# Kernel tuning notes

Measured on AMD Instinct MI355X. Metric: run time of the kernel, lower is better.

Reference implementation:

```python
import jax, jax.numpy as jnp
import numpy as np

B, C, H, W = 32, 512, 32, 32
R = C // 2  # reduced channels for key/prod projections


def setup_inputs() -> dict:
    key = jax.random.key(0)
    ks = jax.random.split(key, 8)
    s_in = 1.0 / np.sqrt(C)
    return {
        "x": jax.random.normal(ks[0], (B, C, H, W), jnp.float32),
        "Wk": jax.random.normal(ks[1], (R, C), jnp.float32) * s_in,
        "bk": jax.random.normal(ks[2], (R,), jnp.float32) * s_in,
        "Wp": jax.random.normal(ks[3], (R, C), jnp.float32) * s_in,
        "bp": jax.random.normal(ks[4], (R,), jnp.float32) * s_in,
        "Wv": jax.random.normal(ks[5], (C, C), jnp.float32) * s_in,
        "bv": jax.random.normal(ks[6], (C,), jnp.float32) * s_in,
        "param": jax.random.normal(ks[7], (1,), jnp.float32),
    }


def _conv1x1(x, Wmat, b):
    # 1x1 conv on NCHW == per-pixel channel matmul
    return jnp.einsum('bchw,oc->bohw', x, Wmat) + b[None, :, None, None]


def reference(x, Wk, bk, Wp, bp, Wv, bv, param):
    b, c, h, w = x.shape
    hw = h * w
    f_key = _conv1x1(x, Wk, bk).reshape(b, -1, hw).transpose(0, 2, 1)  # [B,HW,R]
    f_prod = _conv1x1(x, Wp, bp).reshape(b, -1, hw)                    # [B,R,HW]
    f_value = _conv1x1(x, Wv, bv).reshape(b, -1, hw)                   # [B,C,HW]
    energy = jnp.einsum('bnr,brm->bnm', f_key, f_prod)                 # [B,HW,HW]
    similarity = jax.nn.softmax(energy, axis=-1)
    # bmm(f_value, similarity^T): out[b,c,n] = sum_m f_value[b,c,m] * sim[b,n,m]
    attended = jnp.einsum('bcm,bnm->bcn', f_value, similarity).reshape(b, c, h, w)
    return x + attended * param
```

## Files before the change

kernel.cpp:

```cpp
#include <hip/hip_runtime.h>
#include <hip/hip_bf16.h>

#define BATCH 32
#define CCH   512
#define HWSZ  1024
#define RCH   256

typedef __attribute__((ext_vector_type(8))) _Float16 f16x8;
typedef __attribute__((ext_vector_type(4))) float f32x4;

__device__ __forceinline__ ushort f2h(float f) {
    _Float16 h = (_Float16)f;
    ushort u; __builtin_memcpy(&u, &h, 2);
    return u;
}
__device__ __forceinline__ float h2f(ushort u) {
    _Float16 h; __builtin_memcpy(&h, &u, 2);
    return (float)h;
}

__device__ __forceinline__ void load_lds16(const void* g, void* l) {
    __builtin_amdgcn_global_load_lds((const __attribute__((address_space(1))) void*)g,
                                     (__attribute__((address_space(3))) void*)l,
                                     16, 0, 0);
}

__device__ __forceinline__ void xcd_swizzle(int& bx, int& by, int& bz) {
    int gx = gridDim.x, gy = gridDim.y;
    int n   = gx * gy * gridDim.z;
    int lin = bx + gx * (by + gy * bz);
    int cpx = n >> 3;
    int s = (lin & 7) * cpx + (lin >> 3);
    bx = s % gx; s /= gx;
    by = s % gy;
    bz = s / gy;
}

__global__ __launch_bounds__(256) void k_prep_w(
    const float* __restrict__ Wk, const float* __restrict__ bk,
    const float* __restrict__ Wp, const float* __restrict__ bp,
    const float* __restrict__ Wv,
    ushort* __restrict__ Wkp_h, ushort* __restrict__ Wv_h, float* __restrict__ bias_kp)
{
    int idx = blockIdx.x * 256 + threadIdx.x;
    if (idx < 512 * 512) {
        int o = idx >> 9, c = idx & 511;
        float w = (o < 256) ? Wk[o * 512 + c] : Wp[(o - 256) * 512 + c];
        Wkp_h[idx] = f2h(w);
        Wv_h[idx]  = f2h(Wv[idx]);
        if (c == 0) bias_kp[o] = (o < 256) ? bk[o] : bp[o - 256];
    }
}

__global__ __launch_bounds__(256) void k_transpose(
    const float* __restrict__ x, ushort* __restrict__ xt)
{
    __shared__ float tile[64][65];
    int b  = blockIdx.z;
    int c0 = blockIdx.y * 64;
    int n0 = blockIdx.x * 64;
    const float* xb = x + (size_t)b * CCH * HWSZ;
    int t  = threadIdx.x;
    int tq = t >> 6;
    int tl = t & 63;
    #pragma unroll
    for (int i = 0; i < 16; ++i) {
        int c = i * 4 + tq;
        tile[c][tl] = xb[(size_t)(c0 + c) * HWSZ + n0 + tl];
    }
    __syncthreads();
    ushort* oh = xt + (size_t)b * HWSZ * CCH;
    #pragma unroll
    for (int i = 0; i < 16; ++i) {
        int n = i * 4 + tq;
        oh[(size_t)(n0 + n) * CCH + c0 + tl] = f2h(tile[tl][n]);
    }
}

template<int MODE>
__global__ __launch_bounds__(512, 2) void k_gemm8(
    const ushort* __restrict__ A, const ushort* __restrict__ B,
    int lda, int ldb, long aBatch, long bBatch,
    float* __restrict__ outF, ushort* __restrict__ out16,
    long oBatch, int ldo,
    const float* __restrict__ bias,
    const float* __restrict__ xres, const float* __restrict__ param,
    int NT)
{
    __shared__ ushort lds[2][2][2][8192];
    int bx = blockIdx.x, by = blockIdx.y, bz = blockIdx.z;
    xcd_swizzle(bx, by, bz);
    const int z  = bz;
    const int m0 = bx * 256;
    const int n0 = by * 256;
    const int t    = threadIdx.x;
    const int lane = t & 63;
    const int w    = t >> 6;
    const int wm = w >> 2, wn = w & 3;
    const int l15 = lane & 15;
    const int G   = (lane >> 4) ^ ((lane >> 1) & 3);

    const ushort* Ab = A + (size_t)z * aBatch;
    const ushort* Bb = B + (size_t)z * bBatch;

    const int sr = t >> 2;
    const int sg = (t & 3) ^ ((t >> 3) & 3);

    f32x4 acc[8][4] = {};
    f16x8 a[8], b[2];

#define STAGE(par, op, ks, kt) do {                                          \
        const ushort* gb_ = (op) ? Bb : Ab;                                  \
        int ld_ = (op) ? ldb : lda;                                          \
        int r0_ = (op) ? n0 : m0;                                            \
        size_t src_ = (size_t)(r0_ + sr) * ld_ + (kt) * 64 + (ks) * 32 + sg * 8; \
        load_lds16(gb_ + src_, &lds[par][op][ks][t * 8]);                    \
        load_lds16(gb_ + src_ + (size_t)128 * ld_, &lds[par][op][ks][t * 8 + 4096]); \
    } while (0)

#define LDA_(cur, ks) do {                                                   \
        _Pragma("unroll")                                                    \
        for (int mi = 0; mi < 8; ++mi)                                       \
            a[mi] = *(const f16x8*)&lds[cur][0][ks][(wm * 128 + mi * 16 + l15) * 32 + G * 8]; \
    } while (0)

#define LDB_(cur, ks, nh) do {                                               \
        _Pragma("unroll")                                                    \
        for (int ni = 0; ni < 2; ++ni)                                       \
            b[ni] = *(const f16x8*)&lds[cur][1][ks][(wn * 64 + (nh) * 32 + ni * 16 + l15) * 32 + G * 8]; \
    } while (0)

#define BAR() __builtin_amdgcn_s_barrier()

#define MFMA_BLK(nh) do {                                                    \
        asm volatile("s_waitcnt lgkmcnt(0)" ::: "memory");                   \
        __builtin_amdgcn_sched_barrier(0);                                   \
        __builtin_amdgcn_s_setprio(1);                                       \
        _Pragma("unroll")                                                    \
        for (int mi = 0; mi < 8; ++mi) {                                     \
            acc[mi][(nh)*2+0] = __builtin_amdgcn_mfma_f32_16x16x32_f16(a[mi], b[0], acc[mi][(nh)*2+0], 0, 0, 0); \
            acc[mi][(nh)*2+1] = __builtin_amdgcn_mfma_f32_16x16x32_f16(a[mi], b[1], acc[mi][(nh)*2+1], 0, 0, 0); \
        }                                                                    \
        __builtin_amdgcn_s_setprio(0);                                       \
    } while (0)

    STAGE(0, 0, 0, 0); STAGE(0, 1, 0, 0); STAGE(0, 0, 1, 0); STAGE(0, 1, 1, 0);
    asm volatile("s_waitcnt vmcnt(4)" ::: "memory");
    BAR();

    for (int j = 0; j < NT - 1; ++j) {
        int cur = j & 1, nxt = cur ^ 1;
        STAGE(nxt, 0, 0, j + 1);
        LDA_(cur, 0); LDB_(cur, 0, 0);
        MFMA_BLK(0);
        STAGE(nxt, 1, 0, j + 1);
        LDB_(cur, 0, 1);
        MFMA_BLK(1);
        asm volatile("s_waitcnt vmcnt(4)" ::: "memory");
        BAR();
        STAGE(nxt, 0, 1, j + 1);
        LDA_(cur, 1); LDB_(cur, 1, 0);
        MFMA_BLK(0);
        STAGE(nxt, 1, 1, j + 1);
        LDB_(cur, 1, 1);
        MFMA_BLK(1);
        asm volatile("s_waitcnt vmcnt(4)" ::: "memory");
        BAR();
    }
    {
        int cur = (NT - 1) & 1;
        LDA_(cur, 0); LDB_(cur, 0, 0);
        MFMA_BLK(0);
        LDB_(cur, 0, 1);
        MFMA_BLK(1);
        asm volatile("s_waitcnt vmcnt(0)" ::: "memory");
        BAR();
        LDA_(cur, 1); LDB_(cur, 1, 0);
        MFMA_BLK(0);
        LDB_(cur, 1, 1);
        MFMA_BLK(1);
    }

    const float prm = (MODE == 3) ? param[0] : 0.f;
    #pragma unroll
    for (int mi = 0; mi < 8; ++mi) {
        #pragma unroll
        for (int ni = 0; ni < 4; ++ni) {
            int gc  = n0 + wn * 64 + (ni >> 1) * 32 + (ni & 1) * 16 + l15;
            int gr0 = m0 + wm * 128 + mi * 16 + (lane >> 4) * 4;
            if (MODE == 3) {
                float*       ob = outF + (size_t)z * oBatch;
                const float* xb = xres + (size_t)z * oBatch;
                size_t g = (size_t)gc * ldo + gr0;
                float4 xv = *(const float4*)&xb[g];
                float4 ov;
                ov.x = xv.x + acc[mi][ni][0] * prm;
                ov.y = xv.y + acc[mi][ni][1] * prm;
                ov.z = xv.z + acc[mi][ni][2] * prm;
                ov.w = xv.w + acc[mi][ni][3] * prm;
                *(float4*)&ob[g] = ov;
            } else {
                #pragma unroll
                for (int jj = 0; jj < 4; ++jj) {
                    int gr = gr0 + jj;
                    float v = acc[mi][ni][jj];
                    if (MODE == 0) {
                        v += bias[gc];
                        out16[(size_t)gr * ldo + gc] = f2h(v);
                    } else if (MODE == 1) {
                        v += bias[gr];
                        out16[(size_t)z * oBatch + (size_t)gr * ldo + gc] = f2h(v);
                    } else {
                        out16[(size_t)z * oBatch + (size_t)gr * ldo + gc] = f2h(v);
                    }
                }
            }
        }
    }
#undef STAGE
#undef LDA_
#undef LDB_
#undef BAR
#undef MFMA_BLK
}

__global__ __launch_bounds__(256) void k_softmax(ushort* __restrict__ E)
{
    int blk = blockIdx.x;
    ushort* row = E + (size_t)blk * HWSZ;
    int t = threadIdx.x;
    ushort4 u = *(const ushort4*)&row[t * 4];
    float v0 = h2f(u.x), v1 = h2f(u.y), v2 = h2f(u.z), v3 = h2f(u.w);
    float mx = fmaxf(fmaxf(v0, v1), fmaxf(v2, v3));
    #pragma unroll
    for (int off = 1; off < 64; off <<= 1)
        mx = fmaxf(mx, __shfl_xor(mx, off));
    __shared__ float redm[4];
    __shared__ float reds[4];
    int lane = t & 63, wv = t >> 6;
    if (lane == 0) redm[wv] = mx;
    __syncthreads();
    mx = fmaxf(fmaxf(redm[0], redm[1]), fmaxf(redm[2], redm[3]));
    float e0 = __expf(v0 - mx), e1 = __expf(v1 - mx);
    float e2 = __expf(v2 - mx), e3 = __expf(v3 - mx);
    float s = (e0 + e1) + (e2 + e3);
    #pragma unroll
    for (int off = 1; off < 64; off <<= 1)
        s += __shfl_xor(s, off);
    if (lane == 0) reds[wv] = s;
    __syncthreads();
    s = (reds[0] + reds[1]) + (reds[2] + reds[3]);
    float inv = 1.0f / s;
    ushort4 o;
    o.x = f2h(e0 * inv); o.y = f2h(e1 * inv);
    o.z = f2h(e2 * inv); o.w = f2h(e3 * inv);
    *(ushort4*)&row[t * 4] = o;
}

extern "C" void kernel_launch(void* const* d_in, const int* in_sizes, int n_in,
                              void* d_out, int out_size, void* d_ws, size_t ws_size,
                              hipStream_t stream)
{
    const float* x    = (const float*)d_in[0];
    const float* Wk   = (const float*)d_in[1];
    const float* bk   = (const float*)d_in[2];
    const float* Wp   = (const float*)d_in[3];
    const float* bp   = (const float*)d_in[4];
    const float* Wv   = (const float*)d_in[5];
    const float* bv   = (const float*)d_in[6];
    const float* prm  = (const float*)d_in[7];
    float* out = (float*)d_out;
    char* ws = (char*)d_ws;

    const size_t SZ16 = (size_t)BATCH * HWSZ * CCH * 2;
    ushort* xt    = (ushort*)(ws + 0);
    ushort* KPt   = (ushort*)(ws + SZ16);
    ushort* fv    = (ushort*)(ws + 2 * SZ16);
    ushort* E     = (ushort*)(ws + 3 * SZ16);
    char* wbase   = ws + 3 * SZ16 + (size_t)BATCH * HWSZ * HWSZ * 2;
    ushort* Wkp_h = (ushort*)(wbase);
    ushort* Wv_h  = (ushort*)(wbase + 524288);
    float*  bias_kp = (float*)(wbase + 2 * 524288);

    k_prep_w<<<1024, 256, 0, stream>>>(Wk, bk, Wp, bp, Wv, Wkp_h, Wv_h, bias_kp);
    k_transpose<<<dim3(16, 8, 32), 256, 0, stream>>>(x, xt);

    k_gemm8<0><<<dim3(128, 2, 1), 512, 0, stream>>>(
        xt, Wkp_h, CCH, CCH, 0, 0,
        nullptr, KPt, 0, CCH,
        bias_kp, nullptr, nullptr, CCH / 64);

    k_gemm8<1><<<dim3(2, 4, 32), 512, 0, stream>>>(
        Wv_h, xt, CCH, CCH, 0, (long)HWSZ * CCH,
        nullptr, fv, (long)CCH * HWSZ, HWSZ,
        bv, nullptr, nullptr, CCH / 64);

    k_gemm8<2><<<dim3(4, 4, 32), 512, 0, stream>>>(
        KPt, KPt + RCH, CCH, CCH,
        (long)HWSZ * CCH, (long)HWSZ * CCH,
        nullptr, E, (long)HWSZ * HWSZ, HWSZ,
        nullptr, nullptr, nullptr, RCH / 64);

    k_softmax<<<BATCH * HWSZ, 256, 0, stream>>>(E);

    k_gemm8<3><<<dim3(4, 2, 32), 512, 0, stream>>>(
        E, fv, HWSZ, HWSZ,
        (long)HWSZ * HWSZ, (long)CCH * HWSZ,
        out, nullptr, (long)CCH * HWSZ, HWSZ,
        nullptr, x, prm, HWSZ / 64);
}
```

Measured before the change: 196.5 us.

## Pipeline LDS fragment waits with MFMAs and stage final epilogue through LDS

After: 190.9 us. 1.03x faster.

```diff
diff --git a/kernel.cpp b/kernel.cpp
--- a/kernel.cpp
+++ b/kernel.cpp
@@ -98,7 +98,8 @@
     const int w    = t >> 6;
     const int wm = w >> 2, wn = w & 3;
     const int l15 = lane & 15;
-    const int G   = (lane >> 4) ^ ((lane >> 1) & 3);
+    const int hi  = lane >> 4;
+    const int G   = hi ^ ((lane >> 1) & 3);
 
     const ushort* Ab = A + (size_t)z * aBatch;
     const ushort* Bb = B + (size_t)z * bBatch;
@@ -132,15 +133,27 @@
 
 #define BAR() __builtin_amdgcn_s_barrier()
 
-#define MFMA_BLK(nh) do {                                                    \
-        asm volatile("s_waitcnt lgkmcnt(0)" ::: "memory");                   \
-        __builtin_amdgcn_sched_barrier(0);                                   \
+#define WLG(N) do { asm volatile("s_waitcnt lgkmcnt(" #N ")" ::: "memory");  \
+                    __builtin_amdgcn_sched_barrier(0); } while (0)
+
+#define MM2(mi, nh) do {                                                     \
+        acc[mi][(nh)*2+0] = __builtin_amdgcn_mfma_f32_16x16x32_f16(a[mi], b[0], acc[mi][(nh)*2+0], 0, 0, 0); \
+        acc[mi][(nh)*2+1] = __builtin_amdgcn_mfma_f32_16x16x32_f16(a[mi], b[1], acc[mi][(nh)*2+1], 0, 0, 0); \
+    } while (0)
+
+#define MFMA_PIPE() do {                                                     \
         __builtin_amdgcn_s_setprio(1);                                       \
-        _Pragma("unroll")                                                    \
-        for (int mi = 0; mi < 8; ++mi) {                                     \
-            acc[mi][(nh)*2+0] = __builtin_amdgcn_mfma_f32_16x16x32_f16(a[mi], b[0], acc[mi][(nh)*2+0], 0, 0, 0); \
-            acc[mi][(nh)*2+1] = __builtin_amdgcn_mfma_f32_16x16x32_f16(a[mi], b[1], acc[mi][(nh)*2+1], 0, 0, 0); \
-        }                                                                    \
+        WLG(7); MM2(0, 0); WLG(6); MM2(1, 0); WLG(5); MM2(2, 0);             \
+        WLG(4); MM2(3, 0); WLG(3); MM2(4, 0); WLG(2); MM2(5, 0);             \
+        WLG(1); MM2(6, 0); WLG(0); MM2(7, 0);                                \
+        __builtin_amdgcn_s_setprio(0);                                       \
+    } while (0)
+
+#define MFMA_BLK1() do {                                                     \
+        WLG(0);                                                              \
+        __builtin_amdgcn_s_setprio(1);                                       \
+        MM2(0, 1); MM2(1, 1); MM2(2, 1); MM2(3, 1);                          \
+        MM2(4, 1); MM2(5, 1); MM2(6, 1); MM2(7, 1);                          \
         __builtin_amdgcn_s_setprio(0);                                       \
     } while (0)
 
@@ -151,55 +164,78 @@
     for (int j = 0; j < NT - 1; ++j) {
         int cur = j & 1, nxt = cur ^ 1;
         STAGE(nxt, 0, 0, j + 1);
-        LDA_(cur, 0); LDB_(cur, 0, 0);
-        MFMA_BLK(0);
+        LDB_(cur, 0, 0); LDA_(cur, 0);
+        MFMA_PIPE();
         STAGE(nxt, 1, 0, j + 1);
         LDB_(cur, 0, 1);
-        MFMA_BLK(1);
+        MFMA_BLK1();
         asm volatile("s_waitcnt vmcnt(4)" ::: "memory");
         BAR();
         STAGE(nxt, 0, 1, j + 1);
-        LDA_(cur, 1); LDB_(cur, 1, 0);
-        MFMA_BLK(0);
+        LDB_(cur, 1, 0); LDA_(cur, 1);
+        MFMA_PIPE();
         STAGE(nxt, 1, 1, j + 1);
         LDB_(cur, 1, 1);
-        MFMA_BLK(1);
+        MFMA_BLK1();
         asm volatile("s_waitcnt vmcnt(4)" ::: "memory");
         BAR();
     }
     {
         int cur = (NT - 1) & 1;
-        LDA_(cur, 0); LDB_(cur, 0, 0);
-        MFMA_BLK(0);
+        LDB_(cur, 0, 0); LDA_(cur, 0);
+        MFMA_PIPE();
         LDB_(cur, 0, 1);
-        MFMA_BLK(1);
+        MFMA_BLK1();
         asm volatile("s_waitcnt vmcnt(0)" ::: "memory");
         BAR();
-        LDA_(cur, 1); LDB_(cur, 1, 0);
-        MFMA_BLK(0);
+        LDB_(cur, 1, 0); LDA_(cur, 1);
+        MFMA_PIPE();
         LDB_(cur, 1, 1);
-        MFMA_BLK(1);
-    }
-
-    const float prm = (MODE == 3) ? param[0] : 0.f;
-    #pragma unroll
-    for (int mi = 0; mi < 8; ++mi) {
+        MFMA_BLK1();
+    }
+
+    if (MODE == 3) {
+        float* fbuf = (float*)lds;
+        const float prm = param[0];
+        float*       ob = outF + (size_t)z * oBatch;
+        const float* xb = xres + (size_t)z * oBatch;
         #pragma unroll
-        for (int ni = 0; ni < 4; ++ni) {
-            int gc  = n0 + wn * 64 + (ni >> 1) * 32 + (ni & 1) * 16 + l15;
-            int gr0 = m0 + wm * 128 + mi * 16 + (lane >> 4) * 4;
-            if (MODE == 3) {
-                float*       ob = outF + (size_t)z * oBatch;
-                const float* xb = xres + (size_t)z * oBatch;
-                size_t g = (size_t)gc * ldo + gr0;
+        for (int h = 0; h < 2; ++h) {
+            asm volatile("s_waitcnt lgkmcnt(0)" ::: "memory");
+            BAR();
+            if ((wn >> 1) == h) {
+                #pragma unroll
+                for (int mi = 0; mi < 8; ++mi)
+                    #pragma unroll
+                    for (int ni = 0; ni < 4; ++ni) {
+                        int cc = (wn & 1) * 64 + (ni >> 1) * 32 + (ni & 1) * 16 + l15;
+                        int nn = (wm * 128 + mi * 16 + hi * 4) ^ ((cc & 7) << 2);
+                        *(f32x4*)&fbuf[cc * 256 + nn] = acc[mi][ni];
+                    }
+            }
+            asm volatile("s_waitcnt lgkmcnt(0)" ::: "memory");
+            BAR();
+            #pragma unroll
+            for (int rr = 0; rr < 16; ++rr) {
+                int cc = w * 16 + rr;
+                f32x4 o4 = *(const f32x4*)&fbuf[cc * 256 + ((lane * 4) ^ ((cc & 7) << 2))];
+                size_t g = (size_t)(n0 + h * 128 + cc) * ldo + m0 + lane * 4;
                 float4 xv = *(const float4*)&xb[g];
                 float4 ov;
-                ov.x = xv.x + acc[mi][ni][0] * prm;
-                ov.y = xv.y + acc[mi][ni][1] * prm;
-                ov.z = xv.z + acc[mi][ni][2] * prm;
-                ov.w = xv.w + acc[mi][ni][3] * prm;
+                ov.x = xv.x + o4[0] * prm;
+                ov.y = xv.y + o4[1] * prm;
+                ov.z = xv.z + o4[2] * prm;
+                ov.w = xv.w + o4[3] * prm;
                 *(float4*)&ob[g] = ov;
-            } else {
+            }
+        }
+    } else {
+        #pragma unroll
+        for (int mi = 0; mi < 8; ++mi) {
+            #pragma unroll
+            for (int ni = 0; ni < 4; ++ni) {
+                int gc  = n0 + wn * 64 + (ni >> 1) * 32 + (ni & 1) * 16 + l15;
+                int gr0 = m0 + wm * 128 + mi * 16 + hi * 4;
                 #pragma unroll
                 for (int jj = 0; jj < 4; ++jj) {
                     int gr = gr0 + jj;
@@ -221,7 +257,10 @@
 #undef LDA_
 #undef LDB_
 #undef BAR
-#undef MFMA_BLK
+#undef WLG
+#undef MM2
+#undef MFMA_PIPE
+#undef MFMA_BLK1
 }
 
 __global__ __launch_bounds__(256) void k_softmax(ushort* __restrict__ E)
```
